# Kernel optimization log

Hardware: AMD Instinct MI355X
Metric: run time of the kernel (lower is better)

Reference implementation:

```python
import jax, jax.numpy as jnp
import numpy as np

SEGMENT_LENGTHS = [1024, 2048, 4096]
DILATION_RATES = [1, 2, 4]


def setup_inputs() -> dict:
    key = jax.random.key(0)
    kq, kk, kv = jax.random.split(key, 3)
    shape = (2, 4096, 12, 64)  # (batch, seq_len, num_heads, head_dim)
    return {
        "q": jax.random.normal(kq, shape, dtype=jnp.float32),
        "k": jax.random.normal(kk, shape, dtype=jnp.float32),
        "v": jax.random.normal(kv, shape, dtype=jnp.float32),
        "is_causal": 0,
    }


def _group_attention(qg, kg, vg, L, dil_rate, is_causal, scale):
    # qg/kg/vg: [b, n, hg, d]; block-local attention with block size L.
    # NOTE: the original _get_dilated_indices degenerates to the identity
    # segment slice (i=0 row fills all L indices before truncation), so the
    # dilated gather equals the contiguous segment for any dilation_rate.
    b, n, hg, d = qg.shape
    ns = n // L
    q_ = qg.reshape(b, ns, L, hg, d)
    k_ = kg.reshape(b, ns, L, hg, d)
    v_ = vg.reshape(b, ns, L, hg, d)
    scores = jnp.einsum("bsqhd,bskhd->bshqk", q_, k_) * scale  # [b,ns,hg,L,L]
    if is_causal and dil_rate == 1:
        # causal mask is applied only to segment 0 in the original
        causal = jnp.tril(jnp.ones((L, L), dtype=bool))  # [L,L]
        seg0 = (jnp.arange(ns) == 0)[None, :, None, None, None]  # [1,ns,1,1,1]
        neg = jnp.asarray(jnp.finfo(scores.dtype).min, scores.dtype)
        scores = jnp.where(seg0 & ~causal[None, None, None], neg, scores)
    attn = jax.nn.softmax(scores, axis=-1)
    out = jnp.einsum("bshqk,bskhd->bsqhd", attn, v_)
    return out.reshape(b, n, hg, d)


def reference(q, k, v, is_causal):
    b, n, h, d = q.shape
    num_groups = len(SEGMENT_LENGTHS)
    hg = h // num_groups
    scale = 1.0 / (float(d) ** 0.5)
    outs = []
    for gi, (L, r) in enumerate(zip(SEGMENT_LENGTHS, DILATION_RATES)):
        hs = gi * hg
        he = (gi + 1) * hg if gi < num_groups - 1 else h
        outs.append(
            _group_attention(
                q[:, :, hs:he], k[:, :, hs:he], v[:, :, hs:he],
                L, r, bool(is_causal), scale,
            )
        )
    return jnp.concatenate(outs, axis=2)  # [b, n, h, d]
```

## Files before the change

kernel.cpp:

```cpp
#include <hip/hip_runtime.h>
#include <hip/hip_bf16.h>

typedef __bf16 bf16;
typedef _Float16 f16;
typedef __attribute__((ext_vector_type(2))) __bf16 bf16x2;
typedef __attribute__((ext_vector_type(4))) __bf16 bf16x4;
typedef __attribute__((ext_vector_type(8))) __bf16 bf16x8;
typedef __attribute__((ext_vector_type(4))) _Float16 f16x4;
typedef __attribute__((ext_vector_type(8))) _Float16 f16x8;
typedef __attribute__((ext_vector_type(4))) float f32x4;
typedef __attribute__((ext_vector_type(16))) float f32x16;
typedef __attribute__((ext_vector_type(4))) unsigned u32x4;

#define SW(row, col) ((col) ^ (((row) & 7) << 3))

#define GL16(g, l) __builtin_amdgcn_global_load_lds( \
    (const __attribute__((address_space(1))) void*)(g), \
    (__attribute__((address_space(3))) void*)(l), 16, 0, 0)

static __device__ __forceinline__ unsigned pkbf(float a, float b) {
    bf16x2 t = { (bf16)a, (bf16)b };
    return __builtin_bit_cast(unsigned, t);
}

__global__ __launch_bounds__(256) void prep_fused(
    const float* __restrict__ k, const float* __restrict__ v,
    bf16* __restrict__ Kb, bf16* __restrict__ Vt)
{
    __shared__ bf16 T[64][72];
    const int bid = (int)blockIdx.x;
    const int tid = threadIdx.x;
    if (bid < 6144) {
        const size_t i = ((size_t)bid * 256 + tid) * 4;
        float4 f = *(const float4*)(k + i);
        bf16x4 o = { (bf16)f.x, (bf16)f.y, (bf16)f.z, (bf16)f.w };
        *(bf16x4*)(Kb + i) = o;
        return;
    }
    const int vb  = bid - 6144;
    const int n64 = vb & 63;
    const int bh  = vb >> 6;
    const int b   = bh / 12, h = bh - b * 12;
    {
        const int i  = tid >> 2;
        const int dc = (tid & 3) << 4;
        const float* vp = v + (size_t)(b * 4096 + (n64 << 6) + i) * 768 + h * 64 + dc;
        float tv[16];
#pragma unroll
        for (int j2 = 0; j2 < 4; ++j2) *(float4*)&tv[j2 * 4] = ((const float4*)vp)[j2];
#pragma unroll
        for (int j = 0; j < 16; ++j) T[dc + j][i] = (bf16)tv[j];
    }
    __syncthreads();
    {
        const int d  = tid >> 2;
        const int nc = (tid & 3) << 4;
        bf16* op = Vt + (size_t)(bh * 64 + d) * 4096 + (n64 << 6) + nc;
        *(bf16x8*)op       = *(const bf16x8*)&T[d][nc];
        *(bf16x8*)(op + 8) = *(const bf16x8*)&T[d][nc + 8];
    }
}

__global__ __launch_bounds__(256, 3) void attn_eq(
    const float* __restrict__ q, const bf16* __restrict__ Kb,
    const bf16* __restrict__ Vt, const int* __restrict__ causal_p,
    float* __restrict__ out, f16* __restrict__ Opart, float* __restrict__ lpart)
{
    __shared__ bf16 Ksh[2][64][64];
    __shared__ bf16 Vsh[2][64][64];

    const int tid  = threadIdx.x;
    const int lane = tid & 63;
    const int w    = tid >> 6;
    const int l31  = lane & 31;
    const int h5   = lane >> 5;

    const int bid = (int)blockIdx.x;
    int h, b, qc, so, sp = 0, lbase = 0, oslot = 0;
    bool direct = false, cflag = false;
    if (bid < 1024) {
        h = 8 + (bid >> 8);
        const int r = bid & 255; sp = r >> 6;
        const int r2 = r & 63; b = r2 >> 5; qc = r2 & 31;
        so = sp << 10;
        const int gi = (h - 8) * 64 + b * 32 + qc;
        lbase = gi * 4; oslot = gi * 3 + (sp - 1);
    } else if (bid < 1536) {
        const int i = bid - 1024;
        h = 4 + (i >> 7);
        const int r = i & 127; sp = r >> 6;
        const int r2 = r & 63; b = r2 >> 5; qc = r2 & 31;
        so = ((qc >> 4) << 11) + (sp << 10);
        const int gi = (h - 4) * 64 + b * 32 + qc;
        lbase = 1024 + gi * 2; oslot = 768 + gi;
    } else {
        const int i = bid - 1536;
        h = i >> 6;
        const int r = i & 63; b = r >> 5; qc = r & 31;
        so = (qc >> 3) << 10; direct = true; cflag = true;
    }
    const int q0 = qc << 7;
    const bool causal = cflag && ((qc >> 3) == 0) && (*causal_p != 0);
    const int qg = q0 + (w << 5) + l31;

    const float QS = 0.125f * 1.44269504088896340736f;
    const float* qrp = q + (size_t)(b * 4096 + qg) * 768 + h * 64 + (h5 << 3);
    bf16x8 qf[4];
#pragma unroll
    for (int c = 0; c < 4; ++c) {
        float tq[8];
        *(float4*)&tq[0] = *(const float4*)(qrp + 16 * c);
        *(float4*)&tq[4] = *(const float4*)(qrp + 16 * c + 4);
        bf16x8 t;
#pragma unroll
        for (int j = 0; j < 8; ++j) t[j] = (bf16)(tq[j] * QS);
        qf[c] = t;
    }

    f32x16 o0 = (f32x16)(0.f), o1 = (f32x16)(0.f);
    f32x16 C0 = (f32x16)(-12.0f);
    float lreg = 0.f;

    unsigned loff[8];
#pragma unroll
    for (int c = 0; c < 4; ++c) {
        const int col = (c << 4) + (h5 << 3);
        loff[2 * c + 0] = (unsigned)((l31 * 64 + SW(l31, col)) * 2);
        loff[2 * c + 1] = (unsigned)(((32 + l31) * 64 + SW(32 + l31, col)) * 2);
    }
    const char* KB0 = (const char*)&Ksh[0][0][0];
    const char* VB0 = (const char*)&Vsh[0][0][0];

    const int rK = lane >> 3;
    const int gK = (lane & 7) ^ rK;
    const bf16* kp = Kb + (size_t)(b * 4096 + so + (w << 4) + rK) * 768 + h * 64 + gK * 8;
    const bf16* vp = Vt + (size_t)((b * 12 + h) * 64 + (w << 4) + rK) * 4096 + so + gK * 8;

    {
        bf16* kd = &Ksh[0][w << 4][0];
        bf16* vd = &Vsh[0][w << 4][0];
        GL16(kp, kd); GL16(kp + 8 * 768, kd + 512);
        GL16(vp, vd); GL16(vp + 8 * 4096, vd + 512);
        kp += 64 * 768; vp += 64;
    }

    for (int t = 0; t < 16; ++t) {
        const int buf = t & 1;
        __builtin_amdgcn_s_barrier();
        if (t < 15) {
            bf16* kd = &Ksh[buf ^ 1][w << 4][0];
            bf16* vd = &Vsh[buf ^ 1][w << 4][0];
            GL16(kp, kd); GL16(kp + 8 * 768, kd + 512);
            GL16(vp, vd); GL16(vp + 8 * 4096, vd + 512);
            kp += 64 * 768; vp += 64;
            asm volatile("s_waitcnt vmcnt(4)" ::: "memory");
        } else {
            asm volatile("s_waitcnt vmcnt(0)" ::: "memory");
        }
        __builtin_amdgcn_s_barrier();

        const unsigned bo = (unsigned)(buf << 13);

        f32x16 s0, s1;
        __builtin_amdgcn_s_setprio(1);
#pragma unroll
        for (int c = 0; c < 4; ++c) {
            bf16x8 kf0 = *(const bf16x8*)(KB0 + bo + loff[2 * c + 0]);
            bf16x8 kf1 = *(const bf16x8*)(KB0 + bo + loff[2 * c + 1]);
            if (c == 0) {
                s0 = __builtin_amdgcn_mfma_f32_32x32x16_bf16(kf0, qf[0], C0, 0, 0, 0);
                s1 = __builtin_amdgcn_mfma_f32_32x32x16_bf16(kf1, qf[0], C0, 0, 0, 0);
            } else {
                s0 = __builtin_amdgcn_mfma_f32_32x32x16_bf16(kf0, qf[c], s0, 0, 0, 0);
                s1 = __builtin_amdgcn_mfma_f32_32x32x16_bf16(kf1, qf[c], s1, 0, 0, 0);
            }
        }
        __builtin_amdgcn_s_setprio(0);

        if (causal) {
#pragma unroll
            for (int reg = 0; reg < 16; ++reg) {
                const int kr = (reg & 3) + ((reg >> 2) << 3) + (h5 << 2);
                if (so + (t << 6) + kr > qg)      s0[reg] = -1e30f;
                if (so + (t << 6) + 32 + kr > qg) s1[reg] = -1e30f;
            }
        }

        float rs0 = 0.f, rs1 = 0.f;
#pragma unroll
        for (int reg = 0; reg < 16; ++reg) {
            s0[reg] = __builtin_amdgcn_exp2f(s0[reg]);
            s1[reg] = __builtin_amdgcn_exp2f(s1[reg]);
            rs0 += s0[reg]; rs1 += s1[reg];
        }
        lreg += rs0 + rs1;

        unsigned pk[8][2];
#pragma unroll
        for (int rr = 0; rr < 4; ++rr) {
            pk[rr][0]     = pkbf(s0[4 * rr + 0], s0[4 * rr + 1]);
            pk[rr][1]     = pkbf(s0[4 * rr + 2], s0[4 * rr + 3]);
            pk[4 + rr][0] = pkbf(s1[4 * rr + 0], s1[4 * rr + 1]);
            pk[4 + rr][1] = pkbf(s1[4 * rr + 2], s1[4 * rr + 3]);
        }
        bf16x8 pf[4];
#pragma unroll
        for (int c = 0; c < 4; ++c) {
            unsigned X0 = pk[2 * c][0],     X1 = pk[2 * c][1];
            unsigned Y0 = pk[2 * c + 1][0], Y1 = pk[2 * c + 1][1];
            asm("v_permlane32_swap_b32 %0, %1" : "+v"(X0), "+v"(Y0));
            asm("v_permlane32_swap_b32 %0, %1" : "+v"(X1), "+v"(Y1));
            u32x4 fu = { X0, X1, Y0, Y1 };
            pf[c] = __builtin_bit_cast(bf16x8, fu);
        }

        __builtin_amdgcn_s_setprio(1);
#pragma unroll
        for (int c = 0; c < 4; ++c) {
            bf16x8 vf0 = *(const bf16x8*)(VB0 + bo + loff[2 * c + 0]);
            bf16x8 vf1 = *(const bf16x8*)(VB0 + bo + loff[2 * c + 1]);
            o0 = __builtin_amdgcn_mfma_f32_32x32x16_bf16(vf0, pf[c], o0, 0, 0, 0);
            o1 = __builtin_amdgcn_mfma_f32_32x32x16_bf16(vf1, pf[c], o1, 0, 0, 0);
        }
        __builtin_amdgcn_s_setprio(0);
    }

    const float lt = lreg + __shfl_xor(lreg, 32);
    const int qloc = (w << 5) + l31;
    if (direct) {
        const float inv = 1.0f / lt;
        float* op = out + (size_t)(b * 4096 + q0 + qloc) * 768 + h * 64;
#pragma unroll
        for (int rr = 0; rr < 4; ++rr) {
            const int d0 = (rr << 3) + (h5 << 2);
            float4 a = { o0[4 * rr] * inv, o0[4 * rr + 1] * inv, o0[4 * rr + 2] * inv, o0[4 * rr + 3] * inv };
            float4 c = { o1[4 * rr] * inv, o1[4 * rr + 1] * inv, o1[4 * rr + 2] * inv, o1[4 * rr + 3] * inv };
            *(float4*)&op[d0]      = a;
            *(float4*)&op[32 + d0] = c;
        }
    } else {
        if (h5 == 0) lpart[(size_t)(lbase + sp) * 128 + qloc] = lt;
        if (sp == 0) {
            float* op = out + (size_t)(b * 4096 + q0 + qloc) * 768 + h * 64;
#pragma unroll
            for (int rr = 0; rr < 4; ++rr) {
                const int d0 = (rr << 3) + (h5 << 2);
                float4 a = { o0[4 * rr], o0[4 * rr + 1], o0[4 * rr + 2], o0[4 * rr + 3] };
                float4 c = { o1[4 * rr], o1[4 * rr + 1], o1[4 * rr + 2], o1[4 * rr + 3] };
                *(float4*)&op[d0]      = a;
                *(float4*)&op[32 + d0] = c;
            }
        } else {
            f16* os = Opart + (size_t)oslot * 8192 + qloc * 64;
#pragma unroll
            for (int rr = 0; rr < 4; ++rr) {
                const int d0 = (rr << 3) + (h5 << 2);
                f16x4 a = { (f16)o0[4 * rr], (f16)o0[4 * rr + 1], (f16)o0[4 * rr + 2], (f16)o0[4 * rr + 3] };
                f16x4 c = { (f16)o1[4 * rr], (f16)o1[4 * rr + 1], (f16)o1[4 * rr + 2], (f16)o1[4 * rr + 3] };
                *(f16x4*)&os[d0]      = a;
                *(f16x4*)&os[32 + d0] = c;
            }
        }
    }
}

__global__ __launch_bounds__(256) void reduce_multi(
    const f16* __restrict__ Opart, const float* __restrict__ lpart,
    float* __restrict__ out)
{
    const int g = (int)blockIdx.x;
    int h, b, qc, nsp, lbase, sbase, nslots;
    if (g < 256) {
        h = 8 + (g >> 6); b = (g >> 5) & 1; qc = g & 31;
        nsp = 4; lbase = g * 4; sbase = g * 3; nslots = 3;
    } else {
        const int gi = g - 256;
        h = 4 + (gi >> 6); b = (gi >> 5) & 1; qc = gi & 31;
        nsp = 2; lbase = 1024 + gi * 2; sbase = 768 + gi; nslots = 1;
    }
    const int t = threadIdx.x;
    const int row = t >> 1;
    const int dh = (t & 1) << 5;
    float l = 0.f;
    for (int s = 0; s < nsp; ++s) l += lpart[(size_t)(lbase + s) * 128 + row];
    const float inv = 1.0f / l;
    float* op = out + (size_t)(b * 4096 + (qc << 7) + row) * 768 + h * 64 + dh;
#pragma unroll
    for (int j = 0; j < 32; j += 8) {
        float acc[8];
        float4 a0 = *(const float4*)(op + j);
        float4 a1 = *(const float4*)(op + j + 4);
        acc[0] = a0.x; acc[1] = a0.y; acc[2] = a0.z; acc[3] = a0.w;
        acc[4] = a1.x; acc[5] = a1.y; acc[6] = a1.z; acc[7] = a1.w;
        for (int s = 0; s < nslots; ++s) {
            f16x8 c = *(const f16x8*)(Opart + (size_t)(sbase + s) * 8192 + row * 64 + dh + j);
#pragma unroll
            for (int e = 0; e < 8; ++e) acc[e] += (float)c[e];
        }
        float4 r0 = { acc[0] * inv, acc[1] * inv, acc[2] * inv, acc[3] * inv };
        float4 r1 = { acc[4] * inv, acc[5] * inv, acc[6] * inv, acc[7] * inv };
        *(float4*)(op + j)     = r0;
        *(float4*)(op + j + 4) = r1;
    }
}

__global__ __launch_bounds__(256, 3) void dila_attn32(
    const float* __restrict__ q, const bf16* __restrict__ Kb,
    const bf16* __restrict__ Vt, const int* __restrict__ causal_p,
    float* __restrict__ out, f16* __restrict__ Opart, float* __restrict__ lpart)
{
    __shared__ bf16 Ksh[2][64][64];
    __shared__ bf16 Vsh[2][64][64];

    const int tid  = threadIdx.x;
    const int lane = tid & 63;
    const int w    = tid >> 6;
    const int l31  = lane & 31;
    const int h5   = lane >> 5;

    const int bid = (int)blockIdx.x;
    int h, b, qc, so, nt, sp = 0, gslot = -1;
    bool cflag = false;
    if (bid < 512) {
        h = 8 + (bid >> 7);
        const int r = bid & 127; sp = r >> 6;
        const int r2 = r & 63; b = r2 >> 5; qc = r2 & 31;
        so = sp << 11; nt = 32;
        gslot = (h - 8) * 64 + b * 32 + qc;
    } else if (bid < 768) {
        const int i = bid - 512;
        h = 4 + (i >> 6);
        const int r = i & 63; b = r >> 5; qc = r & 31;
        so = (qc >> 4) << 11; nt = 32;
    } else {
        const int i = bid - 768;
        h = i >> 7;
        const int r = i & 127; sp = r >> 6;
        const int r2 = r & 63; b = r2 >> 5; qc = r2 & 31;
        so = ((qc >> 3) << 10) + (sp << 9); nt = 8; cflag = true;
        gslot = 256 + h * 64 + b * 32 + qc;
    }
    const int q0 = qc << 7;
    const bool causal = cflag && ((qc >> 3) == 0) && (*causal_p != 0);
    const int qg = q0 + (w << 5) + l31;

    const float QS = 0.125f * 1.44269504088896340736f;
    const float* qrp = q + (size_t)(b * 4096 + qg) * 768 + h * 64 + (h5 << 3);
    bf16x8 qf[4];
#pragma unroll
    for (int c = 0; c < 4; ++c) {
        float tq[8];
        *(float4*)&tq[0] = *(const float4*)(qrp + 16 * c);
        *(float4*)&tq[4] = *(const float4*)(qrp + 16 * c + 4);
        bf16x8 t;
#pragma unroll
        for (int j = 0; j < 8; ++j) t[j] = (bf16)(tq[j] * QS);
        qf[c] = t;
    }

    f32x16 o0 = (f32x16)(0.f), o1 = (f32x16)(0.f);
    float lreg = 0.f;

    const int rK = lane >> 3;
    const int gK = (lane & 7) ^ rK;
    const bf16* kp = Kb + (size_t)(b * 4096 + so + (w << 4) + rK) * 768 + h * 64 + gK * 8;
    const bf16* vp = Vt + (size_t)((b * 12 + h) * 64 + (w << 4) + rK) * 4096 + so + gK * 8;

    {
        bf16* kd = &Ksh[0][w << 4][0];
        bf16* vd = &Vsh[0][w << 4][0];
        GL16(kp, kd); GL16(kp + 8 * 768, kd + 512);
        GL16(vp, vd); GL16(vp + 8 * 4096, vd + 512);
        kp += 64 * 768; vp += 64;
    }

    for (int t = 0; t < nt; ++t) {
        const int buf = t & 1;
        __builtin_amdgcn_s_barrier();
        if (t + 1 < nt) {
            bf16* kd = &Ksh[buf ^ 1][w << 4][0];
            bf16* vd = &Vsh[buf ^ 1][w << 4][0];
            GL16(kp, kd); GL16(kp + 8 * 768, kd + 512);
            GL16(vp, vd); GL16(vp + 8 * 4096, vd + 512);
            kp += 64 * 768; vp += 64;
            asm volatile("s_waitcnt vmcnt(4)" ::: "memory");
        } else {
            asm volatile("s_waitcnt vmcnt(0)" ::: "memory");
        }
        __builtin_amdgcn_s_barrier();

        const bf16 (*Kc)[64] = Ksh[buf];
        const bf16 (*Vc)[64] = Vsh[buf];

        f32x16 s0 = (f32x16)(-12.0f), s1 = (f32x16)(-12.0f);
        __builtin_amdgcn_s_setprio(1);
#pragma unroll
        for (int c = 0; c < 4; ++c) {
            const int col = (c << 4) + (h5 << 3);
            bf16x8 kf0 = *(const bf16x8*)&Kc[l31][SW(l31, col)];
            bf16x8 kf1 = *(const bf16x8*)&Kc[32 + l31][SW(32 + l31, col)];
            s0 = __builtin_amdgcn_mfma_f32_32x32x16_bf16(kf0, qf[c], s0, 0, 0, 0);
            s1 = __builtin_amdgcn_mfma_f32_32x32x16_bf16(kf1, qf[c], s1, 0, 0, 0);
        }
        __builtin_amdgcn_s_setprio(0);

        if (causal) {
#pragma unroll
            for (int reg = 0; reg < 16; ++reg) {
                const int kr = (reg & 3) + ((reg >> 2) << 3) + (h5 << 2);
                if (so + (t << 6) + kr > qg)      s0[reg] = -1e30f;
                if (so + (t << 6) + 32 + kr > qg) s1[reg] = -1e30f;
            }
        }

        float p0[16], p1[16], rs = 0.f;
#pragma unroll
        for (int reg = 0; reg < 16; ++reg) {
            p0[reg] = __builtin_amdgcn_exp2f(s0[reg]);
            p1[reg] = __builtin_amdgcn_exp2f(s1[reg]);
            rs += p0[reg] + p1[reg];
        }
        lreg += rs;

        unsigned pk[8][2];
#pragma unroll
        for (int rr = 0; rr < 4; ++rr) {
            pk[rr][0]     = pkbf(p0[4 * rr + 0], p0[4 * rr + 1]);
            pk[rr][1]     = pkbf(p0[4 * rr + 2], p0[4 * rr + 3]);
            pk[4 + rr][0] = pkbf(p1[4 * rr + 0], p1[4 * rr + 1]);
            pk[4 + rr][1] = pkbf(p1[4 * rr + 2], p1[4 * rr + 3]);
        }
        bf16x8 pf[4];
#pragma unroll
        for (int c = 0; c < 4; ++c) {
            unsigned X0 = pk[2 * c][0],     X1 = pk[2 * c][1];
            unsigned Y0 = pk[2 * c + 1][0], Y1 = pk[2 * c + 1][1];
            asm("v_permlane32_swap_b32 %0, %1" : "+v"(X0), "+v"(Y0));
            asm("v_permlane32_swap_b32 %0, %1" : "+v"(X1), "+v"(Y1));
            u32x4 fu = { X0, X1, Y0, Y1 };
            pf[c] = __builtin_bit_cast(bf16x8, fu);
        }

        __builtin_amdgcn_s_setprio(1);
#pragma unroll
        for (int c = 0; c < 4; ++c) {
            const int col = (c << 4) + (h5 << 3);
            bf16x8 vf0 = *(const bf16x8*)&Vc[l31][SW(l31, col)];
            bf16x8 vf1 = *(const bf16x8*)&Vc[32 + l31][SW(32 + l31, col)];
            o0 = __builtin_amdgcn_mfma_f32_32x32x16_bf16(vf0, pf[c], o0, 0, 0, 0);
            o1 = __builtin_amdgcn_mfma_f32_32x32x16_bf16(vf1, pf[c], o1, 0, 0, 0);
        }
        __builtin_amdgcn_s_setprio(0);
    }

    const float lt = lreg + __shfl_xor(lreg, 32);
    const int qloc = (w << 5) + l31;
    if (gslot < 0) {
        const float inv = 1.0f / lt;
        float* op = out + (size_t)(b * 4096 + q0 + qloc) * 768 + h * 64;
#pragma unroll
        for (int rr = 0; rr < 4; ++rr) {
            const int d0 = (rr << 3) + (h5 << 2);
            float4 a = { o0[4 * rr] * inv, o0[4 * rr + 1] * inv, o0[4 * rr + 2] * inv, o0[4 * rr + 3] * inv };
            float4 c = { o1[4 * rr] * inv, o1[4 * rr + 1] * inv, o1[4 * rr + 2] * inv, o1[4 * rr + 3] * inv };
            *(float4*)&op[d0]      = a;
            *(float4*)&op[32 + d0] = c;
        }
    } else if (sp == 0) {
        float* op = out + (size_t)(b * 4096 + q0 + qloc) * 768 + h * 64;
#pragma unroll
        for (int rr = 0; rr < 4; ++rr) {
            const int d0 = (rr << 3) + (h5 << 2);
            float4 a = { o0[4 * rr], o0[4 * rr + 1], o0[4 * rr + 2], o0[4 * rr + 3] };
            float4 c = { o1[4 * rr], o1[4 * rr + 1], o1[4 * rr + 2], o1[4 * rr + 3] };
            *(float4*)&op[d0]      = a;
            *(float4*)&op[32 + d0] = c;
        }
        if (h5 == 0) lpart[gslot * 256 + qloc] = lt;
    } else {
        f16* os = Opart + (size_t)gslot * 8192 + qloc * 64;
#pragma unroll
        for (int rr = 0; rr < 4; ++rr) {
            const int d0 = (rr << 3) + (h5 << 2);
            f16x4 a = { (f16)o0[4 * rr], (f16)o0[4 * rr + 1], (f16)o0[4 * rr + 2], (f16)o0[4 * rr + 3] };
            f16x4 c = { (f16)o1[4 * rr], (f16)o1[4 * rr + 1], (f16)o1[4 * rr + 2], (f16)o1[4 * rr + 3] };
            *(f16x4*)&os[d0]      = a;
            *(f16x4*)&os[32 + d0] = c;
        }
        if (h5 == 0) lpart[gslot * 256 + 128 + qloc] = lt;
    }
}

__global__ __launch_bounds__(256) void reduce_splits(
    const f16* __restrict__ Opart, const float* __restrict__ lpart,
    float* __restrict__ out)
{
    const int g = (int)blockIdx.x;
    int h, b, qc;
    if (g < 256) { h = 8 + (g >> 6); b = (g >> 5) & 1; qc = g & 31; }
    else { const int g2 = g - 256; h = g2 >> 6; b = (g2 >> 5) & 1; qc = g2 & 31; }
    const int t = threadIdx.x;
    const int row = t >> 1;
    const int dh = (t & 1) << 5;
    const f16* s1 = Opart + (size_t)g * 8192 + row * 64 + dh;
    const float inv = 1.0f / (lpart[g * 256 + row] + lpart[g * 256 + 128 + row]);
    float* op = out + (size_t)(b * 4096 + (qc << 7) + row) * 768 + h * 64 + dh;
#pragma unroll
    for (int j = 0; j < 32; j += 8) {
        float4 a0 = *(const float4*)(op + j);
        float4 a1 = *(const float4*)(op + j + 4);
        f16x8 c = *(const f16x8*)(s1 + j);
        float4 r0 = { (a0.x + (float)c[0]) * inv, (a0.y + (float)c[1]) * inv,
                      (a0.z + (float)c[2]) * inv, (a0.w + (float)c[3]) * inv };
        float4 r1 = { (a1.x + (float)c[4]) * inv, (a1.y + (float)c[5]) * inv,
                      (a1.z + (float)c[6]) * inv, (a1.w + (float)c[7]) * inv };
        *(float4*)(op + j)     = r0;
        *(float4*)(op + j + 4) = r1;
    }
}

__global__ __launch_bounds__(256) void dila_attn_legacy(
    const float* __restrict__ q, const float* __restrict__ k,
    const float* __restrict__ v, const int* __restrict__ causal_p,
    float* __restrict__ out)
{
    __shared__ bf16 Ksh[64][64];
    __shared__ bf16 Vsh[64][64];
    __shared__ bf16 Psh[4][16][72];

    const int tid  = threadIdx.x;
    const int lane = tid & 63;
    const int wid  = tid >> 6;
    const int lm   = lane & 15;
    const int lg   = lane >> 4;

    const int h   = 11 - (int)(blockIdx.x >> 7);
    const int rem = (int)(blockIdx.x & 127);
    const int b   = rem >> 6;
    const int qb  = rem & 63;

    const int grp = h >> 2;
    const int L   = 1024 << grp;
    const int q0  = qb << 6;
    const int seg = q0 / L;
    const int kv0 = seg * L;
    const int nt  = L >> 6;
    const bool causal = (grp == 0) && (seg == 0) && (*causal_p != 0);

    const float* qb_p = q   + (size_t)b * 4096 * 768 + h * 64;
    const float* kb_p = k   + (size_t)b * 4096 * 768 + h * 64;
    const float* vb_p = v   + (size_t)b * 4096 * 768 + h * 64;
    float*       ob_p = out + (size_t)b * 4096 * 768 + h * 64;

    const float QSCALE = 0.125f * 1.44269504088896340736f;
    const int qrow = q0 + (wid << 4) + lm;
    const float* qp = qb_p + (size_t)qrow * 768 + (lg << 3);
    bf16x8 qf[2];
#pragma unroll
    for (int kc = 0; kc < 2; ++kc) {
        float tq[8];
        *(float4*)&tq[0] = ((const float4*)(qp + kc * 32))[0];
        *(float4*)&tq[4] = ((const float4*)(qp + kc * 32))[1];
        bf16x8 tt;
#pragma unroll
        for (int j = 0; j < 8; ++j) tt[j] = (bf16)(tq[j] * QSCALE);
        qf[kc] = tt;
    }

    f32x4 o[4];
#pragma unroll
    for (int i = 0; i < 4; ++i) o[i] = (f32x4){0.f, 0.f, 0.f, 0.f};
    float mrun = -1e30f, lrun = 0.f;

    const int sr = tid >> 2;
    const int sc = (tid & 3) << 4;
    const int vbr = tid >> 4;
    const int vbc = tid & 15;

    const float* kp0 = kb_p + (size_t)(kv0 + sr) * 768 + sc;
    const float* vp0 = vb_p + (size_t)(kv0 + (vbr << 2)) * 768 + (vbc << 2);

    for (int t = 0; t < nt; ++t) {
        {
            const float* kp = kp0 + (size_t)t * (64 * 768);
            float tk[16];
#pragma unroll
            for (int i = 0; i < 4; ++i) *(float4*)&tk[4 * i] = ((const float4*)kp)[i];
            bf16x8 c0, c1;
#pragma unroll
            for (int j = 0; j < 8; ++j) { c0[j] = (bf16)tk[j]; c1[j] = (bf16)tk[8 + j]; }
            *(bf16x8*)&Ksh[sr][SW(sr, sc)]     = c0;
            *(bf16x8*)&Ksh[sr][SW(sr, sc + 8)] = c1;
        }
        {
            const float* vp = vp0 + (size_t)t * (64 * 768);
            float4 tv[4];
#pragma unroll
            for (int i = 0; i < 4; ++i) tv[i] = *(const float4*)(vp + (size_t)i * 768);
#pragma unroll
            for (int jc = 0; jc < 4; ++jc) {
                const int d = (vbc << 2) + jc;
                bf16x4 wv = { (bf16)((&tv[0].x)[jc]), (bf16)((&tv[1].x)[jc]),
                              (bf16)((&tv[2].x)[jc]), (bf16)((&tv[3].x)[jc]) };
                *(bf16x4*)&Vsh[d][SW(d, vbr << 2)] = wv;
            }
        }
        __syncthreads();

        f32x4 s[4];
#pragma unroll
        for (int cb = 0; cb < 4; ++cb) {
            f32x4 acc = (f32x4){0.f, 0.f, 0.f, 0.f};
            const int krow = (cb << 4) + lm;
#pragma unroll
            for (int kc = 0; kc < 2; ++kc) {
                bf16x8 kf = *(const bf16x8*)&Ksh[krow][SW(krow, (lg << 3) + (kc << 5))];
                acc = __builtin_amdgcn_mfma_f32_16x16x32_bf16(kf, qf[kc], acc, 0, 0, 0);
            }
            s[cb] = acc;
        }

        if (causal) {
            const int qg = q0 + (wid << 4) + lm;
#pragma unroll
            for (int cb = 0; cb < 4; ++cb) {
                const int kbase = kv0 + (t << 6) + (cb << 4) + (lg << 2);
#pragma unroll
                for (int r = 0; r < 4; ++r)
                    if (kbase + r > qg) s[cb][r] = -1e30f;
            }
        }

        {
            float mx = fmaxf(fmaxf(fmaxf(s[0][0], s[0][1]), fmaxf(s[0][2], s[0][3])),
                             fmaxf(fmaxf(s[1][0], s[1][1]), fmaxf(s[1][2], s[1][3])));
            float mx2 = fmaxf(fmaxf(fmaxf(s[2][0], s[2][1]), fmaxf(s[2][2], s[2][3])),
                              fmaxf(fmaxf(s[3][0], s[3][1]), fmaxf(s[3][2], s[3][3])));
            mx = fmaxf(mx, mx2);
            mx = fmaxf(mx, __shfl_xor(mx, 16));
            mx = fmaxf(mx, __shfl_xor(mx, 32));
            const float mn = fmaxf(mrun, mx);
            const float cr = __builtin_amdgcn_exp2f(mrun - mn);
            mrun = mn;
            float rs = 0.f;
#pragma unroll
            for (int cb = 0; cb < 4; ++cb) {
                f32x4 pp;
#pragma unroll
                for (int r = 0; r < 4; ++r) {
                    pp[r] = __builtin_amdgcn_exp2f(s[cb][r] - mn);
                    rs += pp[r];
                }
                bf16x4 wv = { (bf16)pp[0], (bf16)pp[1], (bf16)pp[2], (bf16)pp[3] };
                *(bf16x4*)&Psh[wid][lm][(cb << 4) + (lg << 2)] = wv;
            }
            rs += __shfl_xor(rs, 16);
            rs += __shfl_xor(rs, 32);
            lrun = lrun * cr + rs;
#pragma unroll
            for (int db = 0; db < 4; ++db)
#pragma unroll
                for (int r = 0; r < 4; ++r) o[db][r] *= cr;
        }

        {
            bf16x8 pfr[2];
#pragma unroll
            for (int kc = 0; kc < 2; ++kc)
                pfr[kc] = *(const bf16x8*)&Psh[wid][lm][(lg << 3) + (kc << 5)];
#pragma unroll
            for (int db = 0; db < 4; ++db) {
                const int vr = (db << 4) + lm;
#pragma unroll
                for (int kc = 0; kc < 2; ++kc) {
                    bf16x8 vf = *(const bf16x8*)&Vsh[vr][SW(vr, (lg << 3) + (kc << 5))];
                    o[db] = __builtin_amdgcn_mfma_f32_16x16x32_bf16(vf, pfr[kc], o[db], 0, 0, 0);
                }
            }
        }
        __syncthreads();
    }

    {
        const float inv = 1.0f / lrun;
        const int orow = q0 + (wid << 4) + lm;
        float* op = ob_p + (size_t)orow * 768 + (lg << 2);
#pragma unroll
        for (int db = 0; db < 4; ++db) {
            float4 wv = { o[db][0] * inv, o[db][1] * inv, o[db][2] * inv, o[db][3] * inv };
            *(float4*)(op + (db << 4)) = wv;
        }
    }
}

extern "C" void kernel_launch(void* const* d_in, const int* in_sizes, int n_in,
                              void* d_out, int out_size, void* d_ws, size_t ws_size,
                              hipStream_t stream) {
    const float* q = (const float*)d_in[0];
    const float* k = (const float*)d_in[1];
    const float* v = (const float*)d_in[2];
    const int* causal_p = (const int*)d_in[3];
    float* out = (float*)d_out;

    const size_t elems = (size_t)2 * 4096 * 12 * 64;
    const size_t kb_b  = elems * sizeof(bf16);
    const size_t vt_b  = elems * sizeof(bf16);

    const size_t opP_b = (size_t)1024 * 8192 * sizeof(f16);
    const size_t lpP_b = (size_t)1536 * 128 * sizeof(float);
    const size_t needP = kb_b + vt_b + opP_b + lpP_b;

    const size_t opF_b = (size_t)512 * 8192 * sizeof(f16);
    const size_t lpF_b = (size_t)512 * 256 * sizeof(float);
    const size_t needF = kb_b + vt_b + opF_b + lpF_b;

    if (ws_size >= needP) {
        bf16* Kb    = (bf16*)d_ws;
        bf16* Vt    = Kb + elems;
        f16*  Opart = (f16*)(Vt + elems);
        float* lpart = (float*)((char*)Opart + opP_b);
        prep_fused<<<dim3(7680), dim3(256), 0, stream>>>(k, v, Kb, Vt);
        attn_eq<<<dim3(1792), dim3(256), 0, stream>>>(q, Kb, Vt, causal_p, out, Opart, lpart);
        reduce_multi<<<dim3(512), dim3(256), 0, stream>>>(Opart, lpart, out);
    } else if (ws_size >= needF) {
        bf16* Kb    = (bf16*)d_ws;
        bf16* Vt    = Kb + elems;
        f16*  Opart = (f16*)(Vt + elems);
        float* lpart = (float*)((char*)Opart + opF_b);
        prep_fused<<<dim3(7680), dim3(256), 0, stream>>>(k, v, Kb, Vt);
        dila_attn32<<<dim3(1280), dim3(256), 0, stream>>>(q, Kb, Vt, causal_p, out, Opart, lpart);
        reduce_splits<<<dim3(512), dim3(256), 0, stream>>>(Opart, lpart, out);
    } else {
        dila_attn_legacy<<<dim3(1536), dim3(256), 0, stream>>>(q, k, v, causal_p, out);
    }
}
```

Before: 109.4 us.

## Process two 32-row query tiles per wave to reuse K/V LDS fragments

Each wave now handles 64 query rows (two 32-row MFMA tiles) instead of 32. Each K and V fragment read from LDS feeds twice as many MFMAs, and the grid is halved to 896 blocks. The partial-output and row-sum buffers and the reduce kernel are re-indexed for 256-row query chunks. In exchange, register pressure roughly doubles (launch bounds drop from 3 to 2 blocks per SM), and fewer blocks may underfill the GPU.

```diff
diff --git a/kernel.cpp b/kernel.cpp
--- a/kernel.cpp
+++ b/kernel.cpp
@@ -61,7 +61,7 @@
     }
 }
 
-__global__ __launch_bounds__(256, 3) void attn_eq(
+__global__ __launch_bounds__(256, 2) void attn_dq(
     const float* __restrict__ q, const bf16* __restrict__ Kb,
     const bf16* __restrict__ Vt, const int* __restrict__ causal_p,
     float* __restrict__ out, f16* __restrict__ Opart, float* __restrict__ lpart)
@@ -78,48 +78,55 @@
     const int bid = (int)blockIdx.x;
     int h, b, qc, so, sp = 0, lbase = 0, oslot = 0;
     bool direct = false, cflag = false;
-    if (bid < 1024) {
-        h = 8 + (bid >> 8);
-        const int r = bid & 255; sp = r >> 6;
-        const int r2 = r & 63; b = r2 >> 5; qc = r2 & 31;
+    if (bid < 512) {
+        h = 8 + (bid >> 7);
+        const int r = bid & 127; sp = r >> 5;
+        const int r2 = r & 31; b = r2 >> 4; qc = r2 & 15;
         so = sp << 10;
-        const int gi = (h - 8) * 64 + b * 32 + qc;
+        const int gi = (h - 8) * 32 + b * 16 + qc;
         lbase = gi * 4; oslot = gi * 3 + (sp - 1);
-    } else if (bid < 1536) {
-        const int i = bid - 1024;
-        h = 4 + (i >> 7);
-        const int r = i & 127; sp = r >> 6;
-        const int r2 = r & 63; b = r2 >> 5; qc = r2 & 31;
-        so = ((qc >> 4) << 11) + (sp << 10);
-        const int gi = (h - 4) * 64 + b * 32 + qc;
-        lbase = 1024 + gi * 2; oslot = 768 + gi;
+    } else if (bid < 768) {
+        const int i = bid - 512;
+        h = 4 + (i >> 6);
+        const int r = i & 63; sp = r >> 5;
+        const int r2 = r & 31; b = r2 >> 4; qc = r2 & 15;
+        so = ((qc >> 3) << 11) + (sp << 10);
+        const int gi = (h - 4) * 32 + b * 16 + qc;
+        lbase = 512 + gi * 2; oslot = 384 + gi;
     } else {
-        const int i = bid - 1536;
-        h = i >> 6;
-        const int r = i & 63; b = r >> 5; qc = r & 31;
-        so = (qc >> 3) << 10; direct = true; cflag = true;
-    }
-    const int q0 = qc << 7;
-    const bool causal = cflag && ((qc >> 3) == 0) && (*causal_p != 0);
-    const int qg = q0 + (w << 5) + l31;
+        const int i = bid - 768;
+        h = i >> 5;
+        const int r = i & 31; b = r >> 4; qc = r & 15;
+        so = (qc >> 2) << 10; direct = true; cflag = true;
+    }
+    const int q0 = qc << 8;
+    const bool causal = cflag && ((qc >> 2) == 0) && (*causal_p != 0);
+    const int qgA = q0 + (w << 6) + l31;
+    const int qgB = qgA + 32;
 
     const float QS = 0.125f * 1.44269504088896340736f;
-    const float* qrp = q + (size_t)(b * 4096 + qg) * 768 + h * 64 + (h5 << 3);
-    bf16x8 qf[4];
-#pragma unroll
-    for (int c = 0; c < 4; ++c) {
-        float tq[8];
-        *(float4*)&tq[0] = *(const float4*)(qrp + 16 * c);
-        *(float4*)&tq[4] = *(const float4*)(qrp + 16 * c + 4);
-        bf16x8 t;
-#pragma unroll
-        for (int j = 0; j < 8; ++j) t[j] = (bf16)(tq[j] * QS);
-        qf[c] = t;
-    }
-
-    f32x16 o0 = (f32x16)(0.f), o1 = (f32x16)(0.f);
+    bf16x8 qfA[4], qfB[4];
+    {
+        const float* qa = q + (size_t)(b * 4096 + qgA) * 768 + h * 64 + (h5 << 3);
+        const float* qb2 = q + (size_t)(b * 4096 + qgB) * 768 + h * 64 + (h5 << 3);
+#pragma unroll
+        for (int c = 0; c < 4; ++c) {
+            float ta[8], tb[8];
+            *(float4*)&ta[0] = *(const float4*)(qa + 16 * c);
+            *(float4*)&ta[4] = *(const float4*)(qa + 16 * c + 4);
+            *(float4*)&tb[0] = *(const float4*)(qb2 + 16 * c);
+            *(float4*)&tb[4] = *(const float4*)(qb2 + 16 * c + 4);
+            bf16x8 va, vb;
+#pragma unroll
+            for (int j = 0; j < 8; ++j) { va[j] = (bf16)(ta[j] * QS); vb[j] = (bf16)(tb[j] * QS); }
+            qfA[c] = va; qfB[c] = vb;
+        }
+    }
+
+    f32x16 oA0 = (f32x16)(0.f), oA1 = (f32x16)(0.f);
+    f32x16 oB0 = (f32x16)(0.f), oB1 = (f32x16)(0.f);
     f32x16 C0 = (f32x16)(-12.0f);
-    float lreg = 0.f;
+    float lregA = 0.f, lregB = 0.f;
 
     unsigned loff[8];
 #pragma unroll
@@ -161,18 +168,22 @@
 
         const unsigned bo = (unsigned)(buf << 13);
 
-        f32x16 s0, s1;
+        f32x16 sA0, sA1, sB0, sB1;
         __builtin_amdgcn_s_setprio(1);
 #pragma unroll
         for (int c = 0; c < 4; ++c) {
             bf16x8 kf0 = *(const bf16x8*)(KB0 + bo + loff[2 * c + 0]);
             bf16x8 kf1 = *(const bf16x8*)(KB0 + bo + loff[2 * c + 1]);
             if (c == 0) {
-                s0 = __builtin_amdgcn_mfma_f32_32x32x16_bf16(kf0, qf[0], C0, 0, 0, 0);
-                s1 = __builtin_amdgcn_mfma_f32_32x32x16_bf16(kf1, qf[0], C0, 0, 0, 0);
+                sA0 = __builtin_amdgcn_mfma_f32_32x32x16_bf16(kf0, qfA[0], C0, 0, 0, 0);
+                sA1 = __builtin_amdgcn_mfma_f32_32x32x16_bf16(kf1, qfA[0], C0, 0, 0, 0);
+                sB0 = __builtin_amdgcn_mfma_f32_32x32x16_bf16(kf0, qfB[0], C0, 0, 0, 0);
+                sB1 = __builtin_amdgcn_mfma_f32_32x32x16_bf16(kf1, qfB[0], C0, 0, 0, 0);
             } else {
-                s0 = __builtin_amdgcn_mfma_f32_32x32x16_bf16(kf0, qf[c], s0, 0, 0, 0);
-                s1 = __builtin_amdgcn_mfma_f32_32x32x16_bf16(kf1, qf[c], s1, 0, 0, 0);
+                sA0 = __builtin_amdgcn_mfma_f32_32x32x16_bf16(kf0, qfA[c], sA0, 0, 0, 0);
+                sA1 = __builtin_amdgcn_mfma_f32_32x32x16_bf16(kf1, qfA[c], sA1, 0, 0, 0);
+                sB0 = __builtin_amdgcn_mfma_f32_32x32x16_bf16(kf0, qfB[c], sB0, 0, 0, 0);
+                sB1 = __builtin_amdgcn_mfma_f32_32x32x16_bf16(kf1, qfB[c], sB1, 0, 0, 0);
             }
         }
         __builtin_amdgcn_s_setprio(0);
@@ -181,37 +192,61 @@
 #pragma unroll
             for (int reg = 0; reg < 16; ++reg) {
                 const int kr = (reg & 3) + ((reg >> 2) << 3) + (h5 << 2);
-                if (so + (t << 6) + kr > qg)      s0[reg] = -1e30f;
-                if (so + (t << 6) + 32 + kr > qg) s1[reg] = -1e30f;
-            }
-        }
-
-        float rs0 = 0.f, rs1 = 0.f;
+                const int kv = so + (t << 6) + kr;
+                if (kv > qgA)      sA0[reg] = -1e30f;
+                if (kv + 32 > qgA) sA1[reg] = -1e30f;
+                if (kv > qgB)      sB0[reg] = -1e30f;
+                if (kv + 32 > qgB) sB1[reg] = -1e30f;
+            }
+        }
+
+        float rsA = 0.f, rsB = 0.f;
 #pragma unroll
         for (int reg = 0; reg < 16; ++reg) {
-            s0[reg] = __builtin_amdgcn_exp2f(s0[reg]);
-            s1[reg] = __builtin_amdgcn_exp2f(s1[reg]);
-            rs0 += s0[reg]; rs1 += s1[reg];
-        }
-        lreg += rs0 + rs1;
-
-        unsigned pk[8][2];
-#pragma unroll
-        for (int rr = 0; rr < 4; ++rr) {
-            pk[rr][0]     = pkbf(s0[4 * rr + 0], s0[4 * rr + 1]);
-            pk[rr][1]     = pkbf(s0[4 * rr + 2], s0[4 * rr + 3]);
-            pk[4 + rr][0] = pkbf(s1[4 * rr + 0], s1[4 * rr + 1]);
-            pk[4 + rr][1] = pkbf(s1[4 * rr + 2], s1[4 * rr + 3]);
-        }
-        bf16x8 pf[4];
-#pragma unroll
-        for (int c = 0; c < 4; ++c) {
-            unsigned X0 = pk[2 * c][0],     X1 = pk[2 * c][1];
-            unsigned Y0 = pk[2 * c + 1][0], Y1 = pk[2 * c + 1][1];
-            asm("v_permlane32_swap_b32 %0, %1" : "+v"(X0), "+v"(Y0));
-            asm("v_permlane32_swap_b32 %0, %1" : "+v"(X1), "+v"(Y1));
-            u32x4 fu = { X0, X1, Y0, Y1 };
-            pf[c] = __builtin_bit_cast(bf16x8, fu);
+            sA0[reg] = __builtin_amdgcn_exp2f(sA0[reg]);
+            sA1[reg] = __builtin_amdgcn_exp2f(sA1[reg]);
+            sB0[reg] = __builtin_amdgcn_exp2f(sB0[reg]);
+            sB1[reg] = __builtin_amdgcn_exp2f(sB1[reg]);
+            rsA += sA0[reg] + sA1[reg];
+            rsB += sB0[reg] + sB1[reg];
+        }
+        lregA += rsA; lregB += rsB;
+
+        bf16x8 pfA[4], pfB[4];
+        {
+            unsigned pk[8][2];
+#pragma unroll
+            for (int rr = 0; rr < 4; ++rr) {
+                pk[rr][0]     = pkbf(sA0[4 * rr + 0], sA0[4 * rr + 1]);
+                pk[rr][1]     = pkbf(sA0[4 * rr + 2], sA0[4 * rr + 3]);
+                pk[4 + rr][0] = pkbf(sA1[4 * rr + 0], sA1[4 * rr + 1]);
+                pk[4 + rr][1] = pkbf(sA1[4 * rr + 2], sA1[4 * rr + 3]);
+            }
+#pragma unroll
+            for (int c = 0; c < 4; ++c) {
+                unsigned X0 = pk[2 * c][0],     X1 = pk[2 * c][1];
+                unsigned Y0 = pk[2 * c + 1][0], Y1 = pk[2 * c + 1][1];
+                asm("v_permlane32_swap_b32 %0, %1" : "+v"(X0), "+v"(Y0));
+                asm("v_permlane32_swap_b32 %0, %1" : "+v"(X1), "+v"(Y1));
+                u32x4 fu = { X0, X1, Y0, Y1 };
+                pfA[c] = __builtin_bit_cast(bf16x8, fu);
+            }
+#pragma unroll
+            for (int rr = 0; rr < 4; ++rr) {
+                pk[rr][0]     = pkbf(sB0[4 * rr + 0], sB0[4 * rr + 1]);
+                pk[rr][1]     = pkbf(sB0[4 * rr + 2], sB0[4 * rr + 3]);
+                pk[4 + rr][0] = pkbf(sB1[4 * rr + 0], sB1[4 * rr + 1]);
+                pk[4 + rr][1] = pkbf(sB1[4 * rr + 2], sB1[4 * rr + 3]);
+            }
+#pragma unroll
+            for (int c = 0; c < 4; ++c) {
+                unsigned X0 = pk[2 * c][0],     X1 = pk[2 * c][1];
+                unsigned Y0 = pk[2 * c + 1][0], Y1 = pk[2 * c + 1][1];
+                asm("v_permlane32_swap_b32 %0, %1" : "+v"(X0), "+v"(Y0));
+                asm("v_permlane32_swap_b32 %0, %1" : "+v"(X1), "+v"(Y1));
+                u32x4 fu = { X0, X1, Y0, Y1 };
+                pfB[c] = __builtin_bit_cast(bf16x8, fu);
+            }
         }
 
         __builtin_amdgcn_s_setprio(1);
@@ -219,72 +254,89 @@
         for (int c = 0; c < 4; ++c) {
             bf16x8 vf0 = *(const bf16x8*)(VB0 + bo + loff[2 * c + 0]);
             bf16x8 vf1 = *(const bf16x8*)(VB0 + bo + loff[2 * c + 1]);
-            o0 = __builtin_amdgcn_mfma_f32_32x32x16_bf16(vf0, pf[c], o0, 0, 0, 0);
-            o1 = __builtin_amdgcn_mfma_f32_32x32x16_bf16(vf1, pf[c], o1, 0, 0, 0);
+            oA0 = __builtin_amdgcn_mfma_f32_32x32x16_bf16(vf0, pfA[c], oA0, 0, 0, 0);
+            oA1 = __builtin_amdgcn_mfma_f32_32x32x16_bf16(vf1, pfA[c], oA1, 0, 0, 0);
+            oB0 = __builtin_amdgcn_mfma_f32_32x32x16_bf16(vf0, pfB[c], oB0, 0, 0, 0);
+            oB1 = __builtin_amdgcn_mfma_f32_32x32x16_bf16(vf1, pfB[c], oB1, 0, 0, 0);
         }
         __builtin_amdgcn_s_setprio(0);
     }
 
-    const float lt = lreg + __shfl_xor(lreg, 32);
-    const int qloc = (w << 5) + l31;
+    const float ltA = lregA + __shfl_xor(lregA, 32);
+    const float ltB = lregB + __shfl_xor(lregB, 32);
+    const int qlocA = (w << 6) + l31;
+    const int qlocB = qlocA + 32;
     if (direct) {
-        const float inv = 1.0f / lt;
-        float* op = out + (size_t)(b * 4096 + q0 + qloc) * 768 + h * 64;
+        const float ia = 1.0f / ltA, ib = 1.0f / ltB;
+        float* opA = out + (size_t)(b * 4096 + q0 + qlocA) * 768 + h * 64;
+        float* opB = out + (size_t)(b * 4096 + q0 + qlocB) * 768 + h * 64;
 #pragma unroll
         for (int rr = 0; rr < 4; ++rr) {
             const int d0 = (rr << 3) + (h5 << 2);
-            float4 a = { o0[4 * rr] * inv, o0[4 * rr + 1] * inv, o0[4 * rr + 2] * inv, o0[4 * rr + 3] * inv };
-            float4 c = { o1[4 * rr] * inv, o1[4 * rr + 1] * inv, o1[4 * rr + 2] * inv, o1[4 * rr + 3] * inv };
-            *(float4*)&op[d0]      = a;
-            *(float4*)&op[32 + d0] = c;
+            float4 a0 = { oA0[4 * rr] * ia, oA0[4 * rr + 1] * ia, oA0[4 * rr + 2] * ia, oA0[4 * rr + 3] * ia };
+            float4 a1 = { oA1[4 * rr] * ia, oA1[4 * rr + 1] * ia, oA1[4 * rr + 2] * ia, oA1[4 * rr + 3] * ia };
+            float4 b0 = { oB0[4 * rr] * ib, oB0[4 * rr + 1] * ib, oB0[4 * rr + 2] * ib, oB0[4 * rr + 3] * ib };
+            float4 b1 = { oB1[4 * rr] * ib, oB1[4 * rr + 1] * ib, oB1[4 * rr + 2] * ib, oB1[4 * rr + 3] * ib };
+            *(float4*)&opA[d0] = a0; *(float4*)&opA[32 + d0] = a1;
+            *(float4*)&opB[d0] = b0; *(float4*)&opB[32 + d0] = b1;
         }
     } else {
-        if (h5 == 0) lpart[(size_t)(lbase + sp) * 128 + qloc] = lt;
+        if (h5 == 0) {
+            lpart[(size_t)(lbase + sp) * 256 + qlocA] = ltA;
+            lpart[(size_t)(lbase + sp) * 256 + qlocB] = ltB;
+        }
         if (sp == 0) {
-            float* op = out + (size_t)(b * 4096 + q0 + qloc) * 768 + h * 64;
+            float* opA = out + (size_t)(b * 4096 + q0 + qlocA) * 768 + h * 64;
+            float* opB = out + (size_t)(b * 4096 + q0 + qlocB) * 768 + h * 64;
 #pragma unroll
             for (int rr = 0; rr < 4; ++rr) {
                 const int d0 = (rr << 3) + (h5 << 2);
-                float4 a = { o0[4 * rr], o0[4 * rr + 1], o0[4 * rr + 2], o0[4 * rr + 3] };
-                float4 c = { o1[4 * rr], o1[4 * rr + 1], o1[4 * rr + 2], o1[4 * rr + 3] };
-                *(float4*)&op[d0]      = a;
-                *(float4*)&op[32 + d0] = c;
+                float4 a0 = { oA0[4 * rr], oA0[4 * rr + 1], oA0[4 * rr + 2], oA0[4 * rr + 3] };
+                float4 a1 = { oA1[4 * rr], oA1[4 * rr + 1], oA1[4 * rr + 2], oA1[4 * rr + 3] };
+                float4 b0 = { oB0[4 * rr], oB0[4 * rr + 1], oB0[4 * rr + 2], oB0[4 * rr + 3] };
+                float4 b1 = { oB1[4 * rr], oB1[4 * rr + 1], oB1[4 * rr + 2], oB1[4 * rr + 3] };
+                *(float4*)&opA[d0] = a0; *(float4*)&opA[32 + d0] = a1;
+                *(float4*)&opB[d0] = b0; *(float4*)&opB[32 + d0] = b1;
             }
         } else {
-            f16* os = Opart + (size_t)oslot * 8192 + qloc * 64;
+            f16* osA = Opart + (size_t)oslot * 16384 + qlocA * 64;
+            f16* osB = Opart + (size_t)oslot * 16384 + qlocB * 64;
 #pragma unroll
             for (int rr = 0; rr < 4; ++rr) {
                 const int d0 = (rr << 3) + (h5 << 2);
-                f16x4 a = { (f16)o0[4 * rr], (f16)o0[4 * rr + 1], (f16)o0[4 * rr + 2], (f16)o0[4 * rr + 3] };
-                f16x4 c = { (f16)o1[4 * rr], (f16)o1[4 * rr + 1], (f16)o1[4 * rr + 2], (f16)o1[4 * rr + 3] };
-                *(f16x4*)&os[d0]      = a;
-                *(f16x4*)&os[32 + d0] = c;
+                f16x4 a0 = { (f16)oA0[4 * rr], (f16)oA0[4 * rr + 1], (f16)oA0[4 * rr + 2], (f16)oA0[4 * rr + 3] };
+                f16x4 a1 = { (f16)oA1[4 * rr], (f16)oA1[4 * rr + 1], (f16)oA1[4 * rr + 2], (f16)oA1[4 * rr + 3] };
+                f16x4 b0 = { (f16)oB0[4 * rr], (f16)oB0[4 * rr + 1], (f16)oB0[4 * rr + 2], (f16)oB0[4 * rr + 3] };
+                f16x4 b1 = { (f16)oB1[4 * rr], (f16)oB1[4 * rr + 1], (f16)oB1[4 * rr + 2], (f16)oB1[4 * rr + 3] };
+                *(f16x4*)&osA[d0] = a0; *(f16x4*)&osA[32 + d0] = a1;
+                *(f16x4*)&osB[d0] = b0; *(f16x4*)&osB[32 + d0] = b1;
             }
         }
     }
 }
 
-__global__ __launch_bounds__(256) void reduce_multi(
+__global__ __launch_bounds__(256) void reduce_dq(
     const f16* __restrict__ Opart, const float* __restrict__ lpart,
     float* __restrict__ out)
 {
-    const int g = (int)blockIdx.x;
+    const int gb   = (int)blockIdx.x >> 1;
+    const int half = (int)blockIdx.x & 1;
     int h, b, qc, nsp, lbase, sbase, nslots;
-    if (g < 256) {
-        h = 8 + (g >> 6); b = (g >> 5) & 1; qc = g & 31;
-        nsp = 4; lbase = g * 4; sbase = g * 3; nslots = 3;
+    if (gb < 128) {
+        h = 8 + (gb >> 5); b = (gb >> 4) & 1; qc = gb & 15;
+        nsp = 4; lbase = gb * 4; sbase = gb * 3; nslots = 3;
     } else {
-        const int gi = g - 256;
-        h = 4 + (gi >> 6); b = (gi >> 5) & 1; qc = gi & 31;
-        nsp = 2; lbase = 1024 + gi * 2; sbase = 768 + gi; nslots = 1;
+        const int gi = gb - 128;
+        h = 4 + (gi >> 5); b = (gi >> 4) & 1; qc = gi & 15;
+        nsp = 2; lbase = 512 + gi * 2; sbase = 384 + gi; nslots = 1;
     }
     const int t = threadIdx.x;
-    const int row = t >> 1;
+    const int row = half * 128 + (t >> 1);
     const int dh = (t & 1) << 5;
     float l = 0.f;
-    for (int s = 0; s < nsp; ++s) l += lpart[(size_t)(lbase + s) * 128 + row];
+    for (int s = 0; s < nsp; ++s) l += lpart[(size_t)(lbase + s) * 256 + row];
     const float inv = 1.0f / l;
-    float* op = out + (size_t)(b * 4096 + (qc << 7) + row) * 768 + h * 64 + dh;
+    float* op = out + (size_t)(b * 4096 + (qc << 8) + row) * 768 + h * 64 + dh;
 #pragma unroll
     for (int j = 0; j < 32; j += 8) {
         float acc[8];
@@ -293,7 +345,7 @@
         acc[0] = a0.x; acc[1] = a0.y; acc[2] = a0.z; acc[3] = a0.w;
         acc[4] = a1.x; acc[5] = a1.y; acc[6] = a1.z; acc[7] = a1.w;
         for (int s = 0; s < nslots; ++s) {
-            f16x8 c = *(const f16x8*)(Opart + (size_t)(sbase + s) * 8192 + row * 64 + dh + j);
+            f16x8 c = *(const f16x8*)(Opart + (size_t)(sbase + s) * 16384 + row * 64 + dh + j);
 #pragma unroll
             for (int e = 0; e < 8; ++e) acc[e] += (float)c[e];
         }
@@ -706,8 +758,8 @@
     const size_t kb_b  = elems * sizeof(bf16);
     const size_t vt_b  = elems * sizeof(bf16);
 
-    const size_t opP_b = (size_t)1024 * 8192 * sizeof(f16);
-    const size_t lpP_b = (size_t)1536 * 128 * sizeof(float);
+    const size_t opP_b = (size_t)512 * 16384 * sizeof(f16);
+    const size_t lpP_b = (size_t)768 * 256 * sizeof(float);
     const size_t needP = kb_b + vt_b + opP_b + lpP_b;
 
     const size_t opF_b = (size_t)512 * 8192 * sizeof(f16);
@@ -720,8 +772,8 @@
         f16*  Opart = (f16*)(Vt + elems);
         float* lpart = (float*)((char*)Opart + opP_b);
         prep_fused<<<dim3(7680), dim3(256), 0, stream>>>(k, v, Kb, Vt);
-        attn_eq<<<dim3(1792), dim3(256), 0, stream>>>(q, Kb, Vt, causal_p, out, Opart, lpart);
-        reduce_multi<<<dim3(512), dim3(256), 0, stream>>>(Opart, lpart, out);
+        attn_dq<<<dim3(896), dim3(256), 0, stream>>>(q, Kb, Vt, causal_p, out, Opart, lpart);
+        reduce_dq<<<dim3(512), dim3(256), 0, stream>>>(Opart, lpart, out);
     } else if (ws_size >= needF) {
         bf16* Kb    = (bf16*)d_ws;
         bf16* Vt    = Kb + elems;
```

Result: slower. 113.3 us (+3.5%).
